# Kernel tuning notes

Hardware: AMD Instinct MI355X
Metric: run time of the kernel (lower is better)

Reference implementation:

```python
import jax, jax.numpy as jnp
import numpy as np

SOFTMAX_SCALE = 0.5  # passed as scalar arg in the original op

def setup_inputs() -> dict:
    key = jax.random.key(0)
    ks = jax.random.split(key, 6)
    B, Sq, H, D, Smax = 8, 1, 32, 128, 4096
    q = jax.random.normal(ks[0], (B, Sq, H, D), dtype=jnp.float32)
    k = jax.random.normal(ks[1], (B, Sq, H, D), dtype=jnp.float32)
    v = jax.random.normal(ks[2], (B, Sq, H, D), dtype=jnp.float32)
    kcache = jax.random.normal(ks[3], (B, Smax, H, D), dtype=jnp.float32)
    vcache = jax.random.normal(ks[4], (B, Smax, H, D), dtype=jnp.float32)
    # current cache occupancy per batch; ensure seqlen + Sq <= Smax
    seqlen = jax.random.randint(ks[5], (B,), 0, Smax - Sq).astype(jnp.int32)
    return {"q": q, "k": k, "v": v, "kcache": kcache, "vcache": vcache, "seqlen": seqlen}

def reference(q, k, v, kcache, vcache, seqlen):
    # Semantics of flash_attn_with_kvcache: append k/v into the cache at
    # offset seqlen[b], then causally attend q over cache[: seqlen[b] + S_new].
    # Causal alignment is bottom-right: query i maps to key position
    # seqlen + S_new - S_q + i.
    B, Sq, H, D = q.shape
    Smax = kcache.shape[1]
    Snew = k.shape[1]
    pos_k = jnp.arange(Smax)          # [Smax]
    pos_q = jnp.arange(Sq)            # [Sq]

    def one_batch(qb, kb, vb, kcb, vcb, sl):
        # qb: [Sq,H,D]; kcb/vcb: [Smax,H,D]; sl: scalar int32
        kc = jax.lax.dynamic_update_slice(kcb, kb, (sl, 0, 0))
        vc = jax.lax.dynamic_update_slice(vcb, vb, (sl, 0, 0))
        scores = jnp.einsum('qhd,khd->hqk', qb, kc) * SOFTMAX_SCALE  # [H,Sq,Smax]
        kmax = sl + Snew - Sq + pos_q                                # [Sq]
        mask = pos_k[None, :] <= kmax[:, None]                       # [Sq,Smax]
        scores = jnp.where(mask[None, :, :], scores, -jnp.inf)
        p = jax.nn.softmax(scores, axis=-1)
        return jnp.einsum('hqk,khd->qhd', p, vc)                     # [Sq,H,D]

    return jax.vmap(one_batch)(q, k, v, kcache, vcache, seqlen)
```

## Files before the change

### kernel.cpp

```cpp
#include <hip/hip_runtime.h>
#include <math.h>

#define B_     8
#define H_     32
#define D_     128
#define SMAX_  4096
#define HD_    (H_ * D_)
#define SCALE  0.5f
#define PSPLIT 128
#define NHG    4
#define PSTRIDE 132

__global__ __launch_bounds__(256, 8)
void attn_partial(const float* __restrict__ q,
                  const float* __restrict__ knew,
                  const float* __restrict__ vnew,
                  const float* __restrict__ kcache,
                  const float* __restrict__ vcache,
                  const int* __restrict__ seqlen,
                  float* __restrict__ ws)
{
    const int blk   = blockIdx.x;
    const int b     = blk & (B_ - 1);
    const int split = (blk >> 3) & (PSPLIT - 1);
    const int hg    = blk >> 10;
    const int t     = threadIdx.x;
    const int h     = hg * 8 + (t >> 5);
    const int dl    = t & 31;
    const int ds    = dl * 4;

    const int sl = seqlen[b];

    const float4 qf = *(const float4*)(q + ((b * H_ + h) * D_ + ds));

    float m = -1e30f, l = 0.f;
    float4 acc = make_float4(0.f, 0.f, 0.f, 0.f);

    const size_t poff  = (size_t)hg * 1024 + (size_t)t * 4;
    const float* kb = kcache + (size_t)b * SMAX_ * HD_ + poff;
    const float* vb = vcache + (size_t)b * SMAX_ * HD_ + poff;
    const size_t pstep = (size_t)HD_ * PSPLIT;

#define STEP1(KP, VP) do {                                                    \
    float4 k0 = *(const float4*)(KP);                                         \
    float4 v0 = *(const float4*)(VP);                                         \
    float s = qf.x*k0.x + qf.y*k0.y + qf.z*k0.z + qf.w*k0.w;                  \
    s += __shfl_xor(s, 1);  s += __shfl_xor(s, 2);  s += __shfl_xor(s, 4);    \
    s += __shfl_xor(s, 8);  s += __shfl_xor(s, 16);                           \
    s *= SCALE;                                                               \
    float mn = fmaxf(m, s);                                                   \
    float sc = __expf(m - mn);                                                \
    float pr = __expf(s - mn);                                                \
    m = mn; l = l * sc + pr;                                                  \
    acc.x = fmaf(pr, v0.x, acc.x * sc);                                       \
    acc.y = fmaf(pr, v0.y, acc.y * sc);                                       \
    acc.z = fmaf(pr, v0.z, acc.z * sc);                                       \
    acc.w = fmaf(pr, v0.w, acc.w * sc);                                       \
} while (0)

    int p = split;
    const float* kp = kb + (size_t)split * HD_;
    const float* vp = vb + (size_t)split * HD_;
    for (; p + PSPLIT < sl; p += 2 * PSPLIT) {
        float4 a0 = *(const float4*)(kp);
        float4 b0 = *(const float4*)(kp + pstep);
        float4 u0 = *(const float4*)(vp);
        float4 w0 = *(const float4*)(vp + pstep);

        float s0 = qf.x*a0.x + qf.y*a0.y + qf.z*a0.z + qf.w*a0.w;
        float s1 = qf.x*b0.x + qf.y*b0.y + qf.z*b0.z + qf.w*b0.w;
        s0 += __shfl_xor(s0, 1);  s0 += __shfl_xor(s0, 2);  s0 += __shfl_xor(s0, 4);
        s0 += __shfl_xor(s0, 8);  s0 += __shfl_xor(s0, 16);
        s1 += __shfl_xor(s1, 1);  s1 += __shfl_xor(s1, 2);  s1 += __shfl_xor(s1, 4);
        s1 += __shfl_xor(s1, 8);  s1 += __shfl_xor(s1, 16);
        s0 *= SCALE; s1 *= SCALE;

        float mn  = fmaxf(m, fmaxf(s0, s1));
        float sc  = __expf(m - mn);
        float pr0 = __expf(s0 - mn);
        float pr1 = __expf(s1 - mn);
        m = mn;
        l = l * sc + pr0 + pr1;
        acc.x = fmaf(pr1, w0.x, fmaf(pr0, u0.x, acc.x * sc));
        acc.y = fmaf(pr1, w0.y, fmaf(pr0, u0.y, acc.y * sc));
        acc.z = fmaf(pr1, w0.z, fmaf(pr0, u0.z, acc.z * sc));
        acc.w = fmaf(pr1, w0.w, fmaf(pr0, u0.w, acc.w * sc));
        kp += 2 * pstep;
        vp += 2 * pstep;
    }
    if (p < sl) {
        STEP1(kp, vp);
    }
    if ((sl & (PSPLIT - 1)) == split) {
        const float* kn = knew + (size_t)b * HD_ + poff;
        const float* vn = vnew + (size_t)b * HD_ + poff;
        STEP1(kn, vn);
    }
#undef STEP1

    float* wsp = ws + (((size_t)b * PSPLIT + split) * H_ + h) * PSTRIDE;
    *(float4*)(wsp + ds) = acc;
    if (dl == 0) { wsp[128] = m; wsp[129] = l; }
}

__global__ __launch_bounds__(128)
void attn_combine(const float* __restrict__ ws, float* __restrict__ out)
{
    const int bh = blockIdx.x;
    const int b  = bh >> 5;
    const int h  = bh & (H_ - 1);
    const int t  = threadIdx.x;

    __shared__ float sm_e[PSPLIT];
    __shared__ float sm_w[2];

    const size_t sstride = (size_t)H_ * PSTRIDE;
    const float* base = ws + ((size_t)b * PSPLIT * H_ + h) * PSTRIDE;

    float mx = -1e30f;
    for (int s = t; s < PSPLIT; s += 128) mx = fmaxf(mx, base[(size_t)s * sstride + 128]);
    #pragma unroll
    for (int off = 1; off < 64; off <<= 1) mx = fmaxf(mx, __shfl_xor(mx, off));
    if ((t & 63) == 0) sm_w[t >> 6] = mx;
    __syncthreads();
    const float mt = fmaxf(sm_w[0], sm_w[1]);
    __syncthreads();

    float le = 0.f;
    for (int s = t; s < PSPLIT; s += 128) {
        const float* p = base + (size_t)s * sstride;
        float ms = p[128], ls = p[129];
        float e = (ls > 0.f) ? __expf(ms - mt) : 0.f;
        sm_e[s] = e;
        le += ls * e;
    }
    #pragma unroll
    for (int off = 1; off < 64; off <<= 1) le += __shfl_xor(le, off);
    if ((t & 63) == 0) sm_w[t >> 6] = le;
    __syncthreads();
    const float lt = sm_w[0] + sm_w[1];

    const float* ab = base + t;
    float a = 0.f;
    #pragma unroll 8
    for (int s = 0; s < PSPLIT; ++s) {
        a += sm_e[s] * ab[(size_t)s * sstride];
    }
    out[bh * D_ + t] = a / lt;
}

extern "C" void kernel_launch(void* const* d_in, const int* in_sizes, int n_in,
                              void* d_out, int out_size, void* d_ws, size_t ws_size,
                              hipStream_t stream) {
    const float* q  = (const float*)d_in[0];
    const float* k  = (const float*)d_in[1];
    const float* v  = (const float*)d_in[2];
    const float* kc = (const float*)d_in[3];
    const float* vc = (const float*)d_in[4];
    const int*   sl = (const int*)d_in[5];
    float* out = (float*)d_out;
    float* ws  = (float*)d_ws;

    attn_partial<<<NHG * PSPLIT * B_, 256, 0, stream>>>(q, k, v, kc, vc, sl, ws);
    attn_combine<<<B_ * H_, 128, 0, stream>>>(ws, out);
}
```

Before: 158.1 us.

## Split KV sequence into contiguous 8-position chunks with all heads per block

Replaces the strided 128-way split over positions and head groups with contiguous chunks of 8 positions. Each block now handles all 32 heads, and each thread covers 16 dims with an 8-lane reduction. Blocks past the sequence length exit early, and the combine pass skips chunks whose weight is zero. This gives contiguous memory access per block and avoids launching idle work. In exchange it uses 512 chunks per batch, which means a much larger workspace and a combine loop that is four times longer and serial per thread.

```diff
diff --git a/kernel.cpp b/kernel.cpp
--- a/kernel.cpp
+++ b/kernel.cpp
@@ -7,100 +7,107 @@
 #define SMAX_  4096
 #define HD_    (H_ * D_)
 #define SCALE  0.5f
-#define PSPLIT 128
-#define NHG    4
+#define CHUNK  8
+#define NCHUNK (SMAX_ / CHUNK)
 #define PSTRIDE 132
 
-__global__ __launch_bounds__(256, 8)
-void attn_partial(const float* __restrict__ q,
-                  const float* __restrict__ knew,
-                  const float* __restrict__ vnew,
-                  const float* __restrict__ kcache,
-                  const float* __restrict__ vcache,
-                  const int* __restrict__ seqlen,
-                  float* __restrict__ ws)
+__global__ void attn_partial(const float* __restrict__ q,
+                             const float* __restrict__ knew,
+                             const float* __restrict__ vnew,
+                             const float* __restrict__ kcache,
+                             const float* __restrict__ vcache,
+                             const int* __restrict__ seqlen,
+                             float* __restrict__ ws)
 {
-    const int blk   = blockIdx.x;
-    const int b     = blk & (B_ - 1);
-    const int split = (blk >> 3) & (PSPLIT - 1);
-    const int hg    = blk >> 10;
-    const int t     = threadIdx.x;
-    const int h     = hg * 8 + (t >> 5);
-    const int dl    = t & 31;
-    const int ds    = dl * 4;
+    const int blk = blockIdx.x;
+    const int b   = blk & (B_ - 1);
+    const int c   = blk >> 3;
+    const int t   = threadIdx.x;
+    const int h   = t >> 3;
+    const int ds  = (t & 7) * 16;
 
-    const int sl = seqlen[b];
+    const int sl    = seqlen[b];
+    const int total = sl + 1;
+    const int cs    = c * CHUNK;
+    const int ce    = min(cs + CHUNK, total);
 
-    const float4 qf = *(const float4*)(q + ((b * H_ + h) * D_ + ds));
+    float* wsp = ws + (((size_t)b * NCHUNK + c) * H_ + h) * PSTRIDE;
+
+    if (cs >= ce) {
+        if ((t & 7) == 0) { wsp[128] = -1e30f; wsp[129] = 0.f; }
+        return;
+    }
+
+    float qf[16];
+    {
+        const float* qp = q + (b * H_ + h) * D_ + ds;
+        float4 t0 = *(const float4*)(qp);
+        float4 t1 = *(const float4*)(qp + 4);
+        float4 t2 = *(const float4*)(qp + 8);
+        float4 t3 = *(const float4*)(qp + 12);
+        qf[0]=t0.x;  qf[1]=t0.y;  qf[2]=t0.z;  qf[3]=t0.w;
+        qf[4]=t1.x;  qf[5]=t1.y;  qf[6]=t1.z;  qf[7]=t1.w;
+        qf[8]=t2.x;  qf[9]=t2.y;  qf[10]=t2.z; qf[11]=t2.w;
+        qf[12]=t3.x; qf[13]=t3.y; qf[14]=t3.z; qf[15]=t3.w;
+    }
 
     float m = -1e30f, l = 0.f;
-    float4 acc = make_float4(0.f, 0.f, 0.f, 0.f);
-
-    const size_t poff  = (size_t)hg * 1024 + (size_t)t * 4;
-    const float* kb = kcache + (size_t)b * SMAX_ * HD_ + poff;
-    const float* vb = vcache + (size_t)b * SMAX_ * HD_ + poff;
-    const size_t pstep = (size_t)HD_ * PSPLIT;
+    float acc[16];
+    #pragma unroll
+    for (int j = 0; j < 16; ++j) acc[j] = 0.f;
 
 #define STEP1(KP, VP) do {                                                    \
     float4 k0 = *(const float4*)(KP);                                         \
+    float4 k1 = *(const float4*)((KP)+4);                                     \
+    float4 k2 = *(const float4*)((KP)+8);                                     \
+    float4 k3 = *(const float4*)((KP)+12);                                    \
     float4 v0 = *(const float4*)(VP);                                         \
-    float s = qf.x*k0.x + qf.y*k0.y + qf.z*k0.z + qf.w*k0.w;                  \
-    s += __shfl_xor(s, 1);  s += __shfl_xor(s, 2);  s += __shfl_xor(s, 4);    \
-    s += __shfl_xor(s, 8);  s += __shfl_xor(s, 16);                           \
+    float4 v1 = *(const float4*)((VP)+4);                                     \
+    float4 v2 = *(const float4*)((VP)+8);                                     \
+    float4 v3 = *(const float4*)((VP)+12);                                    \
+    float s = qf[0]*k0.x+qf[1]*k0.y+qf[2]*k0.z+qf[3]*k0.w                     \
+            + qf[4]*k1.x+qf[5]*k1.y+qf[6]*k1.z+qf[7]*k1.w                     \
+            + qf[8]*k2.x+qf[9]*k2.y+qf[10]*k2.z+qf[11]*k2.w                   \
+            + qf[12]*k3.x+qf[13]*k3.y+qf[14]*k3.z+qf[15]*k3.w;                \
+    s += __shfl_xor(s, 1); s += __shfl_xor(s, 2); s += __shfl_xor(s, 4);      \
     s *= SCALE;                                                               \
     float mn = fmaxf(m, s);                                                   \
     float sc = __expf(m - mn);                                                \
     float pr = __expf(s - mn);                                                \
     m = mn; l = l * sc + pr;                                                  \
-    acc.x = fmaf(pr, v0.x, acc.x * sc);                                       \
-    acc.y = fmaf(pr, v0.y, acc.y * sc);                                       \
-    acc.z = fmaf(pr, v0.z, acc.z * sc);                                       \
-    acc.w = fmaf(pr, v0.w, acc.w * sc);                                       \
+    acc[0]=fmaf(pr,v0.x,acc[0]*sc);  acc[1]=fmaf(pr,v0.y,acc[1]*sc);          \
+    acc[2]=fmaf(pr,v0.z,acc[2]*sc);  acc[3]=fmaf(pr,v0.w,acc[3]*sc);          \
+    acc[4]=fmaf(pr,v1.x,acc[4]*sc);  acc[5]=fmaf(pr,v1.y,acc[5]*sc);          \
+    acc[6]=fmaf(pr,v1.z,acc[6]*sc);  acc[7]=fmaf(pr,v1.w,acc[7]*sc);          \
+    acc[8]=fmaf(pr,v2.x,acc[8]*sc);  acc[9]=fmaf(pr,v2.y,acc[9]*sc);          \
+    acc[10]=fmaf(pr,v2.z,acc[10]*sc);acc[11]=fmaf(pr,v2.w,acc[11]*sc);        \
+    acc[12]=fmaf(pr,v3.x,acc[12]*sc);acc[13]=fmaf(pr,v3.y,acc[13]*sc);        \
+    acc[14]=fmaf(pr,v3.z,acc[14]*sc);acc[15]=fmaf(pr,v3.w,acc[15]*sc);        \
 } while (0)
 
-    int p = split;
-    const float* kp = kb + (size_t)split * HD_;
-    const float* vp = vb + (size_t)split * HD_;
-    for (; p + PSPLIT < sl; p += 2 * PSPLIT) {
-        float4 a0 = *(const float4*)(kp);
-        float4 b0 = *(const float4*)(kp + pstep);
-        float4 u0 = *(const float4*)(vp);
-        float4 w0 = *(const float4*)(vp + pstep);
+    const size_t base = (size_t)b * SMAX_ * HD_ + (size_t)cs * HD_ + (size_t)t * 16;
+    const float* kp = kcache + base;
+    const float* vp = vcache + base;
 
-        float s0 = qf.x*a0.x + qf.y*a0.y + qf.z*a0.z + qf.w*a0.w;
-        float s1 = qf.x*b0.x + qf.y*b0.y + qf.z*b0.z + qf.w*b0.w;
-        s0 += __shfl_xor(s0, 1);  s0 += __shfl_xor(s0, 2);  s0 += __shfl_xor(s0, 4);
-        s0 += __shfl_xor(s0, 8);  s0 += __shfl_xor(s0, 16);
-        s1 += __shfl_xor(s1, 1);  s1 += __shfl_xor(s1, 2);  s1 += __shfl_xor(s1, 4);
-        s1 += __shfl_xor(s1, 8);  s1 += __shfl_xor(s1, 16);
-        s0 *= SCALE; s1 *= SCALE;
-
-        float mn  = fmaxf(m, fmaxf(s0, s1));
-        float sc  = __expf(m - mn);
-        float pr0 = __expf(s0 - mn);
-        float pr1 = __expf(s1 - mn);
-        m = mn;
-        l = l * sc + pr0 + pr1;
-        acc.x = fmaf(pr1, w0.x, fmaf(pr0, u0.x, acc.x * sc));
-        acc.y = fmaf(pr1, w0.y, fmaf(pr0, u0.y, acc.y * sc));
-        acc.z = fmaf(pr1, w0.z, fmaf(pr0, u0.z, acc.z * sc));
-        acc.w = fmaf(pr1, w0.w, fmaf(pr0, u0.w, acc.w * sc));
-        kp += 2 * pstep;
-        vp += 2 * pstep;
+    const int pend = min(ce, sl);
+    for (int p = cs; p < pend; ++p) {
+        STEP1(kp, vp);
+        kp += HD_;
+        vp += HD_;
     }
-    if (p < sl) {
-        STEP1(kp, vp);
-    }
-    if ((sl & (PSPLIT - 1)) == split) {
-        const float* kn = knew + (size_t)b * HD_ + poff;
-        const float* vn = vnew + (size_t)b * HD_ + poff;
+    if (sl >= cs && sl < ce) {
+        const float* kn = knew + (size_t)b * HD_ + t * 16;
+        const float* vn = vnew + (size_t)b * HD_ + t * 16;
         STEP1(kn, vn);
     }
 #undef STEP1
 
-    float* wsp = ws + (((size_t)b * PSPLIT + split) * H_ + h) * PSTRIDE;
-    *(float4*)(wsp + ds) = acc;
-    if (dl == 0) { wsp[128] = m; wsp[129] = l; }
+    if ((t & 7) == 0) { wsp[128] = m; wsp[129] = l; }
+    float* op = wsp + ds;
+    *(float4*)(op)      = make_float4(acc[0],  acc[1],  acc[2],  acc[3]);
+    *(float4*)(op + 4)  = make_float4(acc[4],  acc[5],  acc[6],  acc[7]);
+    *(float4*)(op + 8)  = make_float4(acc[8],  acc[9],  acc[10], acc[11]);
+    *(float4*)(op + 12) = make_float4(acc[12], acc[13], acc[14], acc[15]);
 }
 
 __global__ __launch_bounds__(128)
@@ -111,14 +118,14 @@
     const int h  = bh & (H_ - 1);
     const int t  = threadIdx.x;
 
-    __shared__ float sm_e[PSPLIT];
+    __shared__ float sm_e[NCHUNK];
     __shared__ float sm_w[2];
 
     const size_t sstride = (size_t)H_ * PSTRIDE;
-    const float* base = ws + ((size_t)b * PSPLIT * H_ + h) * PSTRIDE;
+    const float* base = ws + ((size_t)b * NCHUNK * H_ + h) * PSTRIDE;
 
     float mx = -1e30f;
-    for (int s = t; s < PSPLIT; s += 128) mx = fmaxf(mx, base[(size_t)s * sstride + 128]);
+    for (int s = t; s < NCHUNK; s += 128) mx = fmaxf(mx, base[(size_t)s * sstride + 128]);
     #pragma unroll
     for (int off = 1; off < 64; off <<= 1) mx = fmaxf(mx, __shfl_xor(mx, off));
     if ((t & 63) == 0) sm_w[t >> 6] = mx;
@@ -127,7 +134,7 @@
     __syncthreads();
 
     float le = 0.f;
-    for (int s = t; s < PSPLIT; s += 128) {
+    for (int s = t; s < NCHUNK; s += 128) {
         const float* p = base + (size_t)s * sstride;
         float ms = p[128], ls = p[129];
         float e = (ls > 0.f) ? __expf(ms - mt) : 0.f;
@@ -142,9 +149,11 @@
 
     const float* ab = base + t;
     float a = 0.f;
-    #pragma unroll 8
-    for (int s = 0; s < PSPLIT; ++s) {
-        a += sm_e[s] * ab[(size_t)s * sstride];
+    for (int s = 0; s < NCHUNK; ++s) {
+        float e = sm_e[s];
+        if (e != 0.f) {
+            a += e * ab[(size_t)s * sstride];
+        }
     }
     out[bh * D_ + t] = a / lt;
 }
@@ -161,6 +170,6 @@
     float* out = (float*)d_out;
     float* ws  = (float*)d_ws;
 
-    attn_partial<<<NHG * PSPLIT * B_, 256, 0, stream>>>(q, k, v, kc, vc, sl, ws);
+    attn_partial<<<NCHUNK * B_, 256, 0, stream>>>(q, k, v, kc, vc, sl, ws);
     attn_combine<<<B_ * H_, 128, 0, stream>>>(ws, out);
 }
```

After: 398.1 us. 2.52x slower.
